# Kernel tuning notes

Measured on AMD Instinct MI355X. Metric: run time of the kernel, lower is better.

## Reference

```python
import jax, jax.numpy as jnp
import numpy as np

N, E = 50000, 800000
IN, C, H, EDIM = 128, 16, 8, 8  # in_channels, out_channels per head, heads, edge_dim
NEG_SLOPE = 0.2


def setup_inputs() -> dict:
    key = jax.random.key(0)
    ks = jax.random.split(key, 10)
    g = 1.0 / np.sqrt(IN)
    inp = {
        "x": jax.random.normal(ks[0], (N, IN), dtype=jnp.float32),
        "edge_index": jax.random.randint(ks[1], (2, E), 0, N, dtype=jnp.int64),
        "edge_attr": jax.random.normal(ks[2], (E, EDIM), dtype=jnp.float32),
        # GATv2Conv params (share_weights=False): lin_l, lin_r with bias, lin_edge no bias
        "W_l": jax.random.normal(ks[3], (IN, H * C), dtype=jnp.float32) * g,
        "b_l": jnp.zeros((H * C,), dtype=jnp.float32),
        "W_r": jax.random.normal(ks[4], (IN, H * C), dtype=jnp.float32) * g,
        "b_r": jnp.zeros((H * C,), dtype=jnp.float32),
        "W_e": jax.random.normal(ks[5], (EDIM, H * C), dtype=jnp.float32) * (1.0 / np.sqrt(EDIM)),
        "att": jax.random.normal(ks[6], (H, C), dtype=jnp.float32) * (1.0 / np.sqrt(C)),
        "bias": jnp.zeros((H * C,), dtype=jnp.float32),
    }
    return inp


def _gatv2_forward(x, edge_index, edge_attr, W_l, b_l, W_r, b_r, W_e, att, bias):
    n = x.shape[0]
    x_l = (x @ W_l + b_l).reshape(n, H, C)  # source transform
    x_r = (x @ W_r + b_r).reshape(n, H, C)  # target transform

    # add self-loops; edge_attr fill_value='mean' (PyG GATv2Conv default)
    loop = jnp.arange(n, dtype=edge_index.dtype)
    src = jnp.concatenate([edge_index[0], loop])
    dst = jnp.concatenate([edge_index[1], loop])
    loop_attr = jnp.broadcast_to(edge_attr.mean(axis=0, keepdims=True), (n, EDIM))
    e_attr = jnp.concatenate([edge_attr, loop_attr], axis=0)  # [E+N, EDIM]

    e_emb = (e_attr @ W_e).reshape(-1, H, C)  # [E+N, H, C]
    m = x_l[src] + x_r[dst] + e_emb          # gather per edge
    m = jax.nn.leaky_relu(m, NEG_SLOPE)
    logit = jnp.einsum("ehc,hc->eh", m, att)  # [E+N, H]

    # destination-grouped (scatter) softmax
    seg_max = jax.ops.segment_max(logit, dst, num_segments=n)
    expd = jnp.exp(logit - seg_max[dst])
    seg_sum = jax.ops.segment_sum(expd, dst, num_segments=n)
    alpha = expd / (seg_sum[dst] + 1e-16)     # [E+N, H]

    msg = alpha[:, :, None] * x_l[src]        # [E+N, H, C]
    out = jax.ops.segment_sum(msg, dst, num_segments=n)  # [N, H, C]
    return out.reshape(n, H * C) + bias       # concat heads + bias


def reference(x, edge_index, edge_attr, W_l, b_l, W_r, b_r, W_e, att, bias):
    return _gatv2_forward(x, edge_index, edge_attr, W_l, b_l, W_r, b_r, W_e, att, bias)
```

## Files before the change

kernel.cpp:

```cpp
#include <hip/hip_runtime.h>

#define NHEAD 8
#define CH    16
#define HC    128
#define INC   128
#define EDIM  8
#define NEG   0.2f

typedef _Float16 h8 __attribute__((ext_vector_type(8)));
typedef _Float16 h2 __attribute__((ext_vector_type(2)));
typedef float    f4 __attribute__((ext_vector_type(4)));

__device__ __forceinline__ float dot2(h2 a, h2 b, float c) {
#if __has_builtin(__builtin_amdgcn_fdot2)
    return __builtin_amdgcn_fdot2(a, b, c, false);
#else
    return c + (float)a[0] * (float)b[0] + (float)a[1] * (float)b[1];
#endif
}

__global__ __launch_bounds__(256) void k_histpack(
        const float* __restrict__ Wl, const float* __restrict__ Wr,
        const float* __restrict__ We, const float* __restrict__ att,
        _Float16* __restrict__ packed, _Float16* __restrict__ We16, _Float16* __restrict__ att16,
        const int* __restrict__ ei, const float* __restrict__ ea,
        int* __restrict__ cnt, int* __restrict__ rank, float* __restrict__ attr_sum,
        int E) {
    __shared__ float red[4][8];
    if ((int)blockIdx.x < 16) {
        int id = blockIdx.x * 256 + threadIdx.x;
        int l  = id & 63;
        int kb = (id >> 6) & 3;
        int t  = id >> 8;
        int col = t * 16 + (l & 15);
        const float* W = (col < HC) ? Wl : Wr;
        int c = col & 127;
        int kbase = kb * 32 + (l >> 4) * 8;
        _Float16* dst = packed + (size_t)id * 8;
        #pragma unroll
        for (int j = 0; j < 8; ++j) dst[j] = (_Float16)W[(size_t)(kbase + j) * HC + c];
        if (id < 1024) We16[id] = (_Float16)We[id];
        if (id < 128)  att16[id] = (_Float16)att[id];
    } else {
        int t = (blockIdx.x - 16) * 256 + threadIdx.x;
        float av[8] = {0.f, 0.f, 0.f, 0.f, 0.f, 0.f, 0.f, 0.f};
        if (t < E) {
            rank[t] = atomicAdd(&cnt[ei[E + t]], 1);
            float4 a0 = *(const float4*)(ea + (size_t)t * EDIM);
            float4 a1 = *(const float4*)(ea + (size_t)t * EDIM + 4);
            av[0] = a0.x; av[1] = a0.y; av[2] = a0.z; av[3] = a0.w;
            av[4] = a1.x; av[5] = a1.y; av[6] = a1.z; av[7] = a1.w;
        }
        #pragma unroll
        for (int m = 1; m < 64; m <<= 1) {
            #pragma unroll
            for (int k = 0; k < 8; ++k) av[k] += __shfl_xor(av[k], m);
        }
        int lane = threadIdx.x & 63, wid = threadIdx.x >> 6;
        if (lane == 0) {
            #pragma unroll
            for (int k = 0; k < 8; ++k) red[wid][k] = av[k];
        }
        __syncthreads();
        if (threadIdx.x < 8) {
            float s = red[0][threadIdx.x] + red[1][threadIdx.x] + red[2][threadIdx.x] + red[3][threadIdx.x];
            atomicAdd(&attr_sum[threadIdx.x], s);
        }
    }
}

__global__ void k_scan1(const int* __restrict__ cnt, int* __restrict__ off,
                        int* __restrict__ bsum, int N,
                        const float* __restrict__ attr_sum, const float* __restrict__ We,
                        _Float16* __restrict__ loop16, float invE) {
    __shared__ int wpre[16];
    int i = blockIdx.x * 1024 + threadIdx.x;
    int lane = threadIdx.x & 63, wid = threadIdx.x >> 6;
    int v = (i < N) ? cnt[i] : 0;
    int s = v;
    #pragma unroll
    for (int d = 1; d < 64; d <<= 1) {
        int t = __shfl_up(s, d);
        if (lane >= d) s += t;
    }
    if (lane == 63) wpre[wid] = s;
    __syncthreads();
    if (threadIdx.x == 0) {
        int run = 0;
        #pragma unroll
        for (int q = 0; q < 16; ++q) { int t = wpre[q]; wpre[q] = run; run += t; }
        bsum[blockIdx.x] = run;
    }
    __syncthreads();
    if (i <= N) off[i] = wpre[wid] + s - v;

    if (blockIdx.x == 0 && threadIdx.x < HC) {
        int j = threadIdx.x;
        float acc = 0.f;
        #pragma unroll
        for (int d = 0; d < EDIM; ++d) acc += attr_sum[d] * invE * We[d * HC + j];
        loop16[j] = (_Float16)acc;
    }
}

__global__ __launch_bounds__(256) void k_phase2(
        const float* __restrict__ x, const _Float16* __restrict__ packed,
        const float* __restrict__ bl, const float* __restrict__ br,
        _Float16* __restrict__ xh,
        const int* __restrict__ ei, const float* __restrict__ ea,
        const int* __restrict__ off, const int* __restrict__ bsum,
        const int* __restrict__ rank,
        int* __restrict__ esrc, h8* __restrict__ eac,
        int N, int E, int gemmBlocks, int nb) {
    __shared__ _Float16 st[16][264];

    if ((int)blockIdx.x < gemmBlocks) {
        int nb0 = blockIdx.x * 64;
        int w  = threadIdx.x >> 6;
        int l  = threadIdx.x & 63;

        const h8* pk = (const h8*)packed;
        h8 bfrag[4][4];
        #pragma unroll
        for (int t4 = 0; t4 < 4; ++t4)
            #pragma unroll
            for (int kb = 0; kb < 4; ++kb)
                bfrag[t4][kb] = pk[(size_t)(((w * 4 + t4) * 4 + kb) * 64 + l)];

        float bv[4];
        int cl = l & 15;
        #pragma unroll
        for (int t4 = 0; t4 < 4; ++t4) {
            int col = w * 64 + t4 * 16 + cl;
            bv[t4] = (col < HC) ? bl[col] : br[col - HC];
        }

        int g = l >> 4;
        int r0 = g * 4;
        for (int mt = 0; mt < 4; ++mt) {
            int m0 = nb0 + mt * 16;
            if (m0 >= N) break;
            int row = m0 + cl; if (row >= N) row = N - 1;
            const float* xp = x + (size_t)row * INC + g * 8;
            h8 afrag[4];
            #pragma unroll
            for (int kb = 0; kb < 4; ++kb) {
                float4 u = *(const float4*)(xp + kb * 32);
                float4 v = *(const float4*)(xp + kb * 32 + 4);
                h8 a;
                a[0] = (_Float16)u.x; a[1] = (_Float16)u.y; a[2] = (_Float16)u.z; a[3] = (_Float16)u.w;
                a[4] = (_Float16)v.x; a[5] = (_Float16)v.y; a[6] = (_Float16)v.z; a[7] = (_Float16)v.w;
                afrag[kb] = a;
            }
            f4 acc[4];
            #pragma unroll
            for (int t4 = 0; t4 < 4; ++t4) { f4 z = {0.f, 0.f, 0.f, 0.f}; acc[t4] = z; }
            #pragma unroll
            for (int kb = 0; kb < 4; ++kb)
                #pragma unroll
                for (int t4 = 0; t4 < 4; ++t4)
                    acc[t4] = __builtin_amdgcn_mfma_f32_16x16x32_f16(afrag[kb], bfrag[t4][kb], acc[t4], 0, 0, 0);
            #pragma unroll
            for (int t4 = 0; t4 < 4; ++t4) {
                int col = w * 64 + t4 * 16 + cl;
                #pragma unroll
                for (int j = 0; j < 4; ++j)
                    st[r0 + j][col] = (_Float16)(acc[t4][j] + bv[t4]);
            }
            __syncthreads();
            #pragma unroll
            for (int q = 0; q < 2; ++q) {
                int cch = threadIdx.x + 256 * q;
                int r = cch >> 5, ch = (cch & 31) * 8;
                int node = m0 + r;
                if (node < N) *(h8*)(xh + (size_t)node * 256 + ch) = *(const h8*)&st[r][ch];
            }
            __syncthreads();
        }
    } else {
        int lane = threadIdx.x & 63;
        int bv = (lane < nb) ? bsum[lane] : 0;
        int s = bv;
        #pragma unroll
        for (int d = 1; d < 64; d <<= 1) {
            int t = __shfl_up(s, d);
            if (lane >= d) s += t;
        }
        s -= bv;

        int t = (blockIdx.x - gemmBlocks) * 256 + threadIdx.x;
        if (t >= E) return;
        int dst = ei[E + t];
        int pos = off[dst] + __shfl(s, dst >> 10) + rank[t];
        esrc[pos] = ei[t];
        float4 a0 = *(const float4*)(ea + (size_t)t * EDIM);
        float4 a1 = *(const float4*)(ea + (size_t)t * EDIM + 4);
        h8 v;
        v[0] = (_Float16)a0.x; v[1] = (_Float16)a0.y; v[2] = (_Float16)a0.z; v[3] = (_Float16)a0.w;
        v[4] = (_Float16)a1.x; v[5] = (_Float16)a1.y; v[6] = (_Float16)a1.z; v[7] = (_Float16)a1.w;
        eac[pos] = v;
    }
}

__global__ __launch_bounds__(256) void k_gather(
        const int* __restrict__ esrc, const h8* __restrict__ eac,
        const _Float16* __restrict__ We16, const _Float16* __restrict__ att16,
        const _Float16* __restrict__ xh, const _Float16* __restrict__ loop16,
        const float* __restrict__ bias,
        const int* __restrict__ off, const int* __restrict__ bsum,
        float* __restrict__ out, int N, int nb) {
    int wave = (blockIdx.x * blockDim.x + threadIdx.x) >> 6;
    int lane = threadIdx.x & 63;
    if (wave >= N) return;
    int dst = __builtin_amdgcn_readfirstlane(wave);
    int qid = lane >> 4;
    int l   = lane & 15;
    int c0  = l * 8;

    int bv = (lane < nb) ? bsum[lane] : 0;
    int sx = bv;
    #pragma unroll
    for (int d = 1; d < 64; d <<= 1) {
        int t = __shfl_up(sx, d);
        if (lane >= d) sx += t;
    }
    sx -= bv;

    h8 we8[EDIM];
    #pragma unroll
    for (int d = 0; d < EDIM; ++d) we8[d] = *(const h8*)(We16 + d * HC + c0);
    h8 av8 = *(const h8*)(att16 + c0);
    h2 att2[4];
    #pragma unroll
    for (int k = 0; k < 4; ++k) { att2[k][0] = av8[2 * k]; att2[k][1] = av8[2 * k + 1]; }
    h8 lp8 = *(const h8*)(loop16 + c0);
    const h8 z8 = {};
    h8 ng8;
    #pragma unroll
    for (int k = 0; k < 8; ++k) ng8[k] = (_Float16)NEG;

    h8 xr8 = *(const h8*)(xh + (size_t)dst * 256 + HC + c0);

    float accv[8] = {0.f, 0.f, 0.f, 0.f, 0.f, 0.f, 0.f, 0.f};
    float segw = 0.f;

    auto TAIL = [&](h8 m8, h8 x8, bool valid) {
        h8 mp = __builtin_elementwise_max(m8, z8);
        h8 mn = __builtin_elementwise_min(m8, z8);
        m8 = mp + mn * ng8;
        float p = 0.f;
        #pragma unroll
        for (int k = 0; k < 4; ++k) {
            h2 mm; mm[0] = m8[2 * k]; mm[1] = m8[2 * k + 1];
            p = dot2(mm, att2[k], p);
        }
        p += __shfl_xor(p, 1);
        float w = valid ? __expf(p) : 0.f;
        segw += w;
        #pragma unroll
        for (int k = 0; k < 8; ++k) accv[k] += w * (float)x8[k];
    };

    {
        h8 x8 = *(const h8*)(xh + (size_t)dst * 256 + c0);
        TAIL(x8 + xr8 + lp8, x8, qid == 0);
    }

    int q0 = dst >> 10, q1 = (dst + 1) >> 10;
    int beg = off[dst] + __shfl(sx, q0);
    int end = off[dst + 1] + __shfl(sx, q1);
    if (beg < end) {
        int last = end - 1;
        int j = beg + qid; if (j > last) j = last;
        int s0 = esrc[j];
        h8 a0 = eac[j];
        h8 x0 = *(const h8*)(xh + (size_t)s0 * 256 + c0);
        for (int i = beg; i < end; i += 4) {
            int jn = i + 4 + qid; if (jn > last) jn = last;
            int sn = esrc[jn];
            h8 an = eac[jn];
            h8 xn = *(const h8*)(xh + (size_t)sn * 256 + c0);
            h8 m8 = x0 + xr8;
            #pragma unroll
            for (int d = 0; d < EDIM; ++d) {
                h8 ad = {a0[d], a0[d], a0[d], a0[d], a0[d], a0[d], a0[d], a0[d]};
                m8 += ad * we8[d];
            }
            TAIL(m8, x0, (i + qid) < end);
            a0 = an; x0 = xn;
        }
    }

    segw += __shfl_xor(segw, 16); segw += __shfl_xor(segw, 32);
    #pragma unroll
    for (int k = 0; k < 8; ++k) {
        accv[k] += __shfl_xor(accv[k], 16);
        accv[k] += __shfl_xor(accv[k], 32);
    }

    if (qid == 0) {
        float inv = 1.f / (segw + 1e-16f);
        f4 b0 = *(const f4*)(bias + c0), b1 = *(const f4*)(bias + c0 + 4);
        f4 o0, o1;
        o0[0] = accv[0] * inv + b0[0]; o0[1] = accv[1] * inv + b0[1];
        o0[2] = accv[2] * inv + b0[2]; o0[3] = accv[3] * inv + b0[3];
        o1[0] = accv[4] * inv + b1[0]; o1[1] = accv[5] * inv + b1[1];
        o1[2] = accv[6] * inv + b1[2]; o1[3] = accv[7] * inv + b1[3];
        *(f4*)(out + (size_t)dst * HC + c0)     = o0;
        *(f4*)(out + (size_t)dst * HC + c0 + 4) = o1;
    }
}

extern "C" void kernel_launch(void* const* d_in, const int* in_sizes, int n_in,
                              void* d_out, int out_size, void* d_ws, size_t ws_size,
                              hipStream_t stream) {
    int N = in_sizes[0] / INC;
    int E = in_sizes[1] / 2;
    const float* x    = (const float*)d_in[0];
    const int*   ei   = (const int*)d_in[1];
    const float* ea   = (const float*)d_in[2];
    const float* Wl   = (const float*)d_in[3];
    const float* bl   = (const float*)d_in[4];
    const float* Wr   = (const float*)d_in[5];
    const float* br   = (const float*)d_in[6];
    const float* We   = (const float*)d_in[7];
    const float* att  = (const float*)d_in[8];
    const float* bias = (const float*)d_in[9];
    float* out = (float*)d_out;

    _Float16* xh      = (_Float16*)d_ws;
    h8*       eac     = (h8*)(xh + (size_t)N * 256);
    float* attr_sum   = (float*)(eac + E);
    int*   cnt        = (int*)(attr_sum + 8);
    _Float16* loop16  = (_Float16*)(cnt + N);
    _Float16* packed  = loop16 + 128;
    _Float16* We16    = packed + 32768;
    _Float16* att16   = We16 + 1024;
    int*   off        = (int*)(att16 + 128);
    int*   rank       = off + (N + 2);
    int*   esrc       = rank + E;
    int*   bsum       = esrc + E;

    hipMemsetAsync(attr_sum, 0, (8 + (size_t)N) * sizeof(float), stream);

    int histBlocks = (E + 255) / 256;
    k_histpack<<<16 + histBlocks, 256, 0, stream>>>(Wl, Wr, We, att, packed, We16, att16,
                                                    ei, ea, cnt, rank, attr_sum, E);

    int nb = (N + 1 + 1023) / 1024;
    k_scan1<<<nb, 1024, 0, stream>>>(cnt, off, bsum, N, attr_sum, We, loop16, 1.0f / (float)E);

    int gemmBlocks = (N + 63) / 64;
    k_phase2<<<gemmBlocks + histBlocks, 256, 0, stream>>>(x, packed, bl, br, xh,
                                                          ei, ea, off, bsum, rank,
                                                          esrc, eac, N, E, gemmBlocks, nb);

    k_gather<<<((size_t)N * 64 + 255) / 256, 256, 0, stream>>>(esrc, eac, We16, att16, xh, loop16,
                                                               bias, off, bsum, out, N, nb);
}
```

Baseline: 166.0 us.

## Process two destination nodes per wavefront in gather kernel for more ILP

Each wavefront in the gather kernel now handles two consecutive destination nodes, interleaving their edge loops so both nodes' gathers and computations are in flight together. The aim is to hide gather latency with more independent loads per wave and to amortize per-wave setup such as the prefix scan and loading We/att. The cost is more registers and half as many waves, and the loop runs until the longer of the two edge lists is done, so lanes working on the shorter list sit idle.

```diff
diff --git a/kernel.cpp b/kernel.cpp
--- a/kernel.cpp
+++ b/kernel.cpp
@@ -209,10 +209,14 @@
         const float* __restrict__ bias,
         const int* __restrict__ off, const int* __restrict__ bsum,
         float* __restrict__ out, int N, int nb) {
-    int wave = (blockIdx.x * blockDim.x + threadIdx.x) >> 6;
+    int wid = (blockIdx.x * blockDim.x + threadIdx.x) >> 6;
     int lane = threadIdx.x & 63;
-    if (wave >= N) return;
-    int dst = __builtin_amdgcn_readfirstlane(wave);
+    int dstA = wid * 2;
+    if (dstA >= N) return;
+    dstA = __builtin_amdgcn_readfirstlane(dstA);
+    bool hasB = (dstA + 1) < N;
+    int dstB = hasB ? dstA + 1 : dstA;
+
     int qid = lane >> 4;
     int l   = lane & 15;
     int c0  = l * 8;
@@ -239,12 +243,14 @@
     #pragma unroll
     for (int k = 0; k < 8; ++k) ng8[k] = (_Float16)NEG;
 
-    h8 xr8 = *(const h8*)(xh + (size_t)dst * 256 + HC + c0);
-
-    float accv[8] = {0.f, 0.f, 0.f, 0.f, 0.f, 0.f, 0.f, 0.f};
-    float segw = 0.f;
-
-    auto TAIL = [&](h8 m8, h8 x8, bool valid) {
+    h8 xrA = *(const h8*)(xh + (size_t)dstA * 256 + HC + c0);
+    h8 xrB = *(const h8*)(xh + (size_t)dstB * 256 + HC + c0);
+
+    float accA[8] = {0.f, 0.f, 0.f, 0.f, 0.f, 0.f, 0.f, 0.f};
+    float accB[8] = {0.f, 0.f, 0.f, 0.f, 0.f, 0.f, 0.f, 0.f};
+    float segA = 0.f, segB = 0.f;
+
+    auto TAIL = [&](h8 m8, h8 x8, bool valid, float (&av)[8], float &sw) {
         h8 mp = __builtin_elementwise_max(m8, z8);
         h8 mn = __builtin_elementwise_min(m8, z8);
         m8 = mp + mn * ng8;
@@ -256,58 +262,101 @@
         }
         p += __shfl_xor(p, 1);
         float w = valid ? __expf(p) : 0.f;
-        segw += w;
-        #pragma unroll
-        for (int k = 0; k < 8; ++k) accv[k] += w * (float)x8[k];
+        sw += w;
+        #pragma unroll
+        for (int k = 0; k < 8; ++k) av[k] += w * (float)x8[k];
     };
 
     {
-        h8 x8 = *(const h8*)(xh + (size_t)dst * 256 + c0);
-        TAIL(x8 + xr8 + lp8, x8, qid == 0);
-    }
-
-    int q0 = dst >> 10, q1 = (dst + 1) >> 10;
-    int beg = off[dst] + __shfl(sx, q0);
-    int end = off[dst + 1] + __shfl(sx, q1);
-    if (beg < end) {
-        int last = end - 1;
-        int j = beg + qid; if (j > last) j = last;
-        int s0 = esrc[j];
-        h8 a0 = eac[j];
-        h8 x0 = *(const h8*)(xh + (size_t)s0 * 256 + c0);
-        for (int i = beg; i < end; i += 4) {
-            int jn = i + 4 + qid; if (jn > last) jn = last;
-            int sn = esrc[jn];
-            h8 an = eac[jn];
-            h8 xn = *(const h8*)(xh + (size_t)sn * 256 + c0);
-            h8 m8 = x0 + xr8;
-            #pragma unroll
-            for (int d = 0; d < EDIM; ++d) {
-                h8 ad = {a0[d], a0[d], a0[d], a0[d], a0[d], a0[d], a0[d], a0[d]};
-                m8 += ad * we8[d];
+        h8 x8 = *(const h8*)(xh + (size_t)dstA * 256 + c0);
+        TAIL(x8 + xrA + lp8, x8, qid == 0, accA, segA);
+    }
+    {
+        h8 x8 = *(const h8*)(xh + (size_t)dstB * 256 + c0);
+        TAIL(x8 + xrB + lp8, x8, hasB && qid == 0, accB, segB);
+    }
+
+    int begA = off[dstA] + __shfl(sx, dstA >> 10);
+    int endA = off[dstA + 1] + __shfl(sx, (dstA + 1) >> 10);
+    int begB = begA, endB = begA;
+    if (hasB) {
+        begB = endA;
+        endB = off[dstA + 2] + __shfl(sx, (dstA + 2) >> 10);
+    }
+
+    if (begA < endA || begB < endB) {
+        int lastA = endA - 1, lastB = endB - 1;
+        bool okA = endA > begA, okB = endB > begB;
+        auto IDXA = [&](int i) { int j = i + qid; j = (j > lastA) ? lastA : j; return okA ? j : 0; };
+        auto IDXB = [&](int i) { int j = i + qid; j = (j > lastB) ? lastB : j; return okB ? j : 0; };
+
+        int jA = IDXA(begA), jB = IDXB(begB);
+        int sA = esrc[jA]; h8 aA = eac[jA];
+        int sB = esrc[jB]; h8 aB = eac[jB];
+        h8 xA = *(const h8*)(xh + (size_t)sA * 256 + c0);
+        h8 xB = *(const h8*)(xh + (size_t)sB * 256 + c0);
+
+        int iA = begA, iB = begB;
+        while (iA < endA || iB < endB) {
+            int jnA = IDXA(iA + 4), jnB = IDXB(iB + 4);
+            int snA = esrc[jnA]; h8 anA = eac[jnA];
+            int snB = esrc[jnB]; h8 anB = eac[jnB];
+            h8 xnA = *(const h8*)(xh + (size_t)snA * 256 + c0);
+            h8 xnB = *(const h8*)(xh + (size_t)snB * 256 + c0);
+
+            {
+                h8 m8 = xA + xrA;
+                #pragma unroll
+                for (int d = 0; d < EDIM; ++d) {
+                    h8 ad = {aA[d], aA[d], aA[d], aA[d], aA[d], aA[d], aA[d], aA[d]};
+                    m8 += ad * we8[d];
+                }
+                TAIL(m8, xA, (iA + qid) < endA, accA, segA);
             }
-            TAIL(m8, x0, (i + qid) < end);
-            a0 = an; x0 = xn;
-        }
-    }
-
-    segw += __shfl_xor(segw, 16); segw += __shfl_xor(segw, 32);
+            {
+                h8 m8 = xB + xrB;
+                #pragma unroll
+                for (int d = 0; d < EDIM; ++d) {
+                    h8 ad = {aB[d], aB[d], aB[d], aB[d], aB[d], aB[d], aB[d], aB[d]};
+                    m8 += ad * we8[d];
+                }
+                TAIL(m8, xB, (iB + qid) < endB, accB, segB);
+            }
+            aA = anA; xA = xnA; aB = anB; xB = xnB;
+            iA += 4; iB += 4;
+        }
+    }
+
+    segA += __shfl_xor(segA, 16); segA += __shfl_xor(segA, 32);
+    segB += __shfl_xor(segB, 16); segB += __shfl_xor(segB, 32);
     #pragma unroll
     for (int k = 0; k < 8; ++k) {
-        accv[k] += __shfl_xor(accv[k], 16);
-        accv[k] += __shfl_xor(accv[k], 32);
+        accA[k] += __shfl_xor(accA[k], 16); accA[k] += __shfl_xor(accA[k], 32);
+        accB[k] += __shfl_xor(accB[k], 16); accB[k] += __shfl_xor(accB[k], 32);
     }
 
     if (qid == 0) {
-        float inv = 1.f / (segw + 1e-16f);
         f4 b0 = *(const f4*)(bias + c0), b1 = *(const f4*)(bias + c0 + 4);
-        f4 o0, o1;
-        o0[0] = accv[0] * inv + b0[0]; o0[1] = accv[1] * inv + b0[1];
-        o0[2] = accv[2] * inv + b0[2]; o0[3] = accv[3] * inv + b0[3];
-        o1[0] = accv[4] * inv + b1[0]; o1[1] = accv[5] * inv + b1[1];
-        o1[2] = accv[6] * inv + b1[2]; o1[3] = accv[7] * inv + b1[3];
-        *(f4*)(out + (size_t)dst * HC + c0)     = o0;
-        *(f4*)(out + (size_t)dst * HC + c0 + 4) = o1;
+        {
+            float inv = 1.f / (segA + 1e-16f);
+            f4 o0, o1;
+            o0[0] = accA[0] * inv + b0[0]; o0[1] = accA[1] * inv + b0[1];
+            o0[2] = accA[2] * inv + b0[2]; o0[3] = accA[3] * inv + b0[3];
+            o1[0] = accA[4] * inv + b1[0]; o1[1] = accA[5] * inv + b1[1];
+            o1[2] = accA[6] * inv + b1[2]; o1[3] = accA[7] * inv + b1[3];
+            *(f4*)(out + (size_t)dstA * HC + c0)     = o0;
+            *(f4*)(out + (size_t)dstA * HC + c0 + 4) = o1;
+        }
+        if (hasB) {
+            float inv = 1.f / (segB + 1e-16f);
+            f4 o0, o1;
+            o0[0] = accB[0] * inv + b0[0]; o0[1] = accB[1] * inv + b0[1];
+            o0[2] = accB[2] * inv + b0[2]; o0[3] = accB[3] * inv + b0[3];
+            o1[0] = accB[4] * inv + b1[0]; o1[1] = accB[5] * inv + b1[1];
+            o1[2] = accB[6] * inv + b1[2]; o1[3] = accB[7] * inv + b1[3];
+            *(f4*)(out + (size_t)dstB * HC + c0)     = o0;
+            *(f4*)(out + (size_t)dstB * HC + c0 + 4) = o1;
+        }
     }
 }
 
@@ -355,6 +404,7 @@
                                                           ei, ea, off, bsum, rank,
                                                           esrc, eac, N, E, gemmBlocks, nb);
 
-    k_gather<<<((size_t)N * 64 + 255) / 256, 256, 0, stream>>>(esrc, eac, We16, att16, xh, loop16,
-                                                               bias, off, bsum, out, N, nb);
-}
+    int waves = (N + 1) / 2;
+    k_gather<<<((size_t)waves * 64 + 255) / 256, 256, 0, stream>>>(esrc, eac, We16, att16, xh, loop16,
+                                                                   bias, off, bsum, out, N, nb);
+}
```

New measurement: 163.2 us, median of 2. About the same (-1.7%).
